# Optimization experiments

Measured on AMD Instinct MI355X. Metric: run time of the kernel, lower is better.

The kernel has to match this reference:

```python
import jax, jax.numpy as jnp
import numpy as np

N_NODES = 50000
N_EDGES = 800000
DIM_IN = 64
DIM_H = 32
HEADS = 4
NUM_CLASSES = 10
NEG_SLOPE = 0.2  # DGL GATv2Conv default negative_slope


def _gatv2_layer(x, W_src, b_src, W_dst, b_dst, attn, src, dst):
    """DGL GATv2Conv (share_weights=False, eval mode so feat_drop is identity).
    x: [N, F_in]; attn: [H, D]; returns [N, H, D]."""
    N = x.shape[0]
    H, D = attn.shape
    fs = (x @ W_src + b_src).reshape(N, H, D)  # source projection
    fd = (x @ W_dst + b_dst).reshape(N, H, D)  # destination projection
    # per-edge additive attention: leaky_relu(fs[u] + fd[v]) . attn  -> [E, H]
    e = jax.nn.leaky_relu(fs[src] + fd[dst], NEG_SLOPE)  # [E, H, D]
    s = jnp.einsum('ehd,hd->eh', e, attn)  # [E, H]
    # edge softmax over incoming edges of each destination node
    smax = jax.lax.stop_gradient(
        jax.ops.segment_max(s, dst, num_segments=N))  # [N, H]
    es = jnp.exp(s - smax[dst])
    denom = jax.ops.segment_sum(es, dst, num_segments=N)  # [N, H]
    alpha = es / denom[dst]
    # weighted scatter-aggregate of source features
    out = jax.ops.segment_sum(alpha[:, :, None] * fs[src], dst, num_segments=N)
    return out  # [N, H, D]


def setup_inputs() -> dict:
    key = jax.random.key(0)
    ks = jax.random.split(key, 16)
    sc = 0.05
    inp = {
        'g_feats': jax.random.normal(ks[0], (N_NODES, DIM_IN), jnp.float32),
        'edge_src': jax.random.randint(ks[1], (N_EDGES,), 0, N_NODES, jnp.int32),
        'edge_dst': jax.random.randint(ks[2], (N_EDGES,), 0, N_NODES, jnp.int32),
        # input embedding Linear(dim_in, dim_h)
        'W_in': jax.random.normal(ks[3], (DIM_IN, DIM_H), jnp.float32) * sc,
        'b_in': jnp.zeros((DIM_H,), jnp.float32),
        # GATv2 layer 1: Linear(dim_h, heads*dim_h) for src/dst + attn [H, D]
        'W1_src': jax.random.normal(ks[4], (DIM_H, HEADS * DIM_H), jnp.float32) * sc,
        'b1_src': jnp.zeros((HEADS * DIM_H,), jnp.float32),
        'W1_dst': jax.random.normal(ks[5], (DIM_H, HEADS * DIM_H), jnp.float32) * sc,
        'b1_dst': jnp.zeros((HEADS * DIM_H,), jnp.float32),
        'attn1': jax.random.normal(ks[6], (HEADS, DIM_H), jnp.float32) * sc,
        # GATv2 layer 2
        'W2_src': jax.random.normal(ks[7], (DIM_H, HEADS * DIM_H), jnp.float32) * sc,
        'b2_src': jnp.zeros((HEADS * DIM_H,), jnp.float32),
        'W2_dst': jax.random.normal(ks[8], (DIM_H, HEADS * DIM_H), jnp.float32) * sc,
        'b2_dst': jnp.zeros((HEADS * DIM_H,), jnp.float32),
        'attn2': jax.random.normal(ks[9], (HEADS, DIM_H), jnp.float32) * sc,
        # MLP head: Linear(dim_h, dim_h) -> relu -> (dropout: eval) -> Linear(dim_h, num_classes)
        'Wh1': jax.random.normal(ks[10], (DIM_H, DIM_H), jnp.float32) * sc,
        'bh1': jnp.zeros((DIM_H,), jnp.float32),
        'Wh2': jax.random.normal(ks[11], (DIM_H, NUM_CLASSES), jnp.float32) * sc,
        'bh2': jnp.zeros((NUM_CLASSES,), jnp.float32),
    }
    return inp


def reference(g_feats, W_in, b_in,
              W1_src, b1_src, W1_dst, b1_dst, attn1,
              W2_src, b2_src, W2_dst, b2_dst, attn2,
              Wh1, bh1, Wh2, bh2,
              edge_src, edge_dst):
    x = g_feats @ W_in + b_in  # input embedding, [N, dim_h]
    h = _gatv2_layer(x, W1_src, b1_src, W1_dst, b1_dst, attn1, edge_src, edge_dst)
    h = jax.nn.relu(h.mean(axis=1))  # mean over heads -> [N, dim_h]
    h = _gatv2_layer(h, W2_src, b2_src, W2_dst, b2_dst, attn2, edge_src, edge_dst)
    h = h.mean(axis=1)  # [N, dim_h]
    # dgl.readout_nodes(op='mean') over the single graph -> [1, dim_h]
    g = h.mean(axis=0, keepdims=True)
    g = jax.nn.relu(g @ Wh1 + bh1)  # head (dropout inactive in eval)
    logits = g @ Wh2 + bh2
    return jax.nn.softmax(logits, axis=-1)  # [1, num_classes]
```

## Files before the change

kernel.cpp:

```cpp
#include <hip/hip_runtime.h>
#include <hip/hip_bf16.h>

#define N_NODES 50000
#define N_EDGES 800000
#define DIM_IN 64
#define DIM_H 32
#define HEADS 4
#define NCLS 10
#define NEG 0.2f
#define NBUCK 196


__global__ void k_bhist(const int* __restrict__ dst, int* __restrict__ bh) {
    __shared__ int lh[NBUCK];
    for (int i = threadIdx.x; i < NBUCK; i += 256) lh[i] = 0;
    __syncthreads();
    int base = blockIdx.x * 1024 + threadIdx.x;
#pragma unroll
    for (int r = 0; r < 4; r++) {
        int e = base + r * 256;
        if (e < N_EDGES) atomicAdd(&lh[dst[e] >> 8], 1);
    }
    __syncthreads();
    for (int i = threadIdx.x; i < NBUCK; i += 256) {
        int c = lh[i];
        if (c) atomicAdd(&bh[i], c);
    }
}

__global__ void k_bscan(const int* __restrict__ bh, int* __restrict__ bbase,
                        int* __restrict__ gcur) {
    __shared__ int s[256];
    int t = threadIdx.x;
    int v = (t < NBUCK) ? bh[t] : 0;
    s[t] = v;
    __syncthreads();
    for (int off = 1; off < 256; off <<= 1) {
        int u = (t >= off) ? s[t - off] : 0;
        __syncthreads();
        s[t] += u;
        __syncthreads();
    }
    int excl = s[t] - v;
    if (t < NBUCK) {
        bbase[t] = excl;
        gcur[t] = excl;
    }
    if (t == 0) bbase[NBUCK] = N_EDGES;
}

__global__ void k_bin(const int* __restrict__ src, const int* __restrict__ dst,
                      int* __restrict__ gcur, unsigned* __restrict__ stage) {
    __shared__ int lh[NBUCK], chunk[NBUCK];
    int t = threadIdx.x;
    for (int i = t; i < NBUCK; i += 256) lh[i] = 0;
    __syncthreads();
    int e0 = blockIdx.x * 4096;
    unsigned pk[16];
    int bk[16];
#pragma unroll
    for (int r = 0; r < 16; r++) {
        int e = e0 + r * 256 + t;
        bool ok = e < N_EDGES;
        int s = ok ? src[e] : 0;
        int d = ok ? dst[e] : 0;
        bk[r] = ok ? (d >> 8) : -1;
        pk[r] = (unsigned)s | ((unsigned)(d & 255) << 16);
        if (ok) atomicAdd(&lh[bk[r]], 1);
    }
    __syncthreads();
    for (int i = t; i < NBUCK; i += 256) {
        int c = lh[i];
        chunk[i] = c ? atomicAdd(&gcur[i], c) : 0;
        lh[i] = 0;
    }
    __syncthreads();
#pragma unroll
    for (int r = 0; r < 16; r++) {
        if (bk[r] >= 0) {
            int lp = atomicAdd(&lh[bk[r]], 1);
            stage[chunk[bk[r]] + lp] = pk[r];
        }
    }
}

__global__ void k_csr(const unsigned* __restrict__ stage, const int* __restrict__ bbase,
                      int* __restrict__ row, int* __restrict__ adj) {
    __shared__ int lcnt[256], lcur[256], sc[256];
    int b = blockIdx.x, t = threadIdx.x;
    int s0 = bbase[b], s1 = bbase[b + 1];
    lcnt[t] = 0;
    __syncthreads();
    for (int i = s0 + t; i < s1; i += 256) atomicAdd(&lcnt[stage[i] >> 16], 1);
    __syncthreads();
    int v = lcnt[t];
    sc[t] = v;
    __syncthreads();
    for (int off = 1; off < 256; off <<= 1) {
        int u = (t >= off) ? sc[t - off] : 0;
        __syncthreads();
        sc[t] += u;
        __syncthreads();
    }
    int excl = sc[t] - v;
    int n = b * 256 + t;
    if (n < N_NODES) row[n] = s0 + excl;
    if (b == NBUCK - 1 && t == 0) row[N_NODES] = N_EDGES;
    lcur[t] = s0 + excl;
    __syncthreads();
    for (int i = s0 + t; i < s1; i += 256) {
        unsigned p = stage[i];
        int pos = atomicAdd(&lcur[p >> 16], 1);
        adj[pos] = (int)(p & 0xFFFFu);
    }
}


__device__ __forceinline__ unsigned short f2bf(float v) {
    unsigned u = __builtin_bit_cast(unsigned, v);
    u += 0x7FFFu + ((u >> 16) & 1u);
    return (unsigned short)(u >> 16);
}
__device__ __forceinline__ float bf2f(unsigned short h) {
    return __builtin_bit_cast(float, (unsigned)h << 16);
}

__global__ __launch_bounds__(256, 1) void k_fused1(
    const float* __restrict__ gf, const float* __restrict__ W_in,
    const float* __restrict__ b_in, const float* __restrict__ W1s,
    const float* __restrict__ b1s, const float* __restrict__ W1d,
    const float* __restrict__ b1d, unsigned short* __restrict__ fsh,
    float* __restrict__ fd) {
    __shared__ float4 xb[4][2][8];
    int lane = threadIdx.x & 63;
    int wvl = threadIdx.x >> 6;
    int wave = (blockIdx.x * 256 + threadIdx.x) >> 6;
    int c = lane & 31, h = lane >> 5;
    int n0 = wave * 16;
    if (n0 >= N_NODES) return;
    float wi[32];
#pragma unroll
    for (int k = 0; k < 32; k++) wi[k] = W_in[(h * 32 + k) * DIM_H + c];
    float bc = b_in[c];
    const float4* Wb = (lane < 32) ? (const float4*)W1s : (const float4*)W1d;
    const float4* bb = (lane < 32) ? (const float4*)b1s : (const float4*)b1d;
    float4 w[32];
#pragma unroll
    for (int k = 0; k < 32; k++) w[k] = Wb[k * 32 + c];
    float4 bias = bb[c];
#pragma unroll 2
    for (int i = 0; i < 16; i++) {
        int nu = __builtin_amdgcn_readfirstlane(n0 + i);
        const float4* gr = (const float4*)(gf + (size_t)nu * DIM_IN + h * 32);
        float a1 = 0.f;
#pragma unroll
        for (int k4 = 0; k4 < 8; k4++) {
            float4 xv = gr[k4];
            a1 += xv.x * wi[k4 * 4 + 0];
            a1 += xv.y * wi[k4 * 4 + 1];
            a1 += xv.z * wi[k4 * 4 + 2];
            a1 += xv.w * wi[k4 * 4 + 3];
        }
        a1 += __shfl_xor(a1, 32, 64);
        if (lane < 32) ((float*)&xb[wvl][i & 1][0])[c] = a1 + bc;
        float4 acc = bias;
#pragma unroll
        for (int k4 = 0; k4 < 8; k4++) {
            float4 xv = xb[wvl][i & 1][k4];
#pragma unroll
            for (int j = 0; j < 4; j++) {
                float xk = (j == 0) ? xv.x : (j == 1) ? xv.y : (j == 2) ? xv.z : xv.w;
                float4 wk = w[k4 * 4 + j];
                acc.x += xk * wk.x;
                acc.y += xk * wk.y;
                acc.z += xk * wk.z;
                acc.w += xk * wk.w;
            }
        }
        if (lane < 32) {
            ushort4 o;
            o.x = f2bf(acc.x);
            o.y = f2bf(acc.y);
            o.z = f2bf(acc.z);
            o.w = f2bf(acc.w);
            *(ushort4*)&fsh[(size_t)nu * 128 + c * 4] = o;
        } else {
            *(float4*)&fd[(size_t)nu * 128 + c * 4] = acc;
        }
    }
}

__global__ __launch_bounds__(256, 1) void k_proj(
    const float* __restrict__ x, const float* __restrict__ Wsrc,
    const float* __restrict__ bsrc, const float* __restrict__ Wdst,
    const float* __restrict__ bdst, unsigned short* __restrict__ fsh,
    float* __restrict__ fd) {
    int lane = threadIdx.x & 63;
    int wave = (blockIdx.x * 256 + threadIdx.x) >> 6;
    int cl = lane & 31;
    int n0 = wave * 16;
    if (n0 >= N_NODES) return;
    const float4* Wb = (lane < 32) ? (const float4*)Wsrc : (const float4*)Wdst;
    const float4* bb = (lane < 32) ? (const float4*)bsrc : (const float4*)bdst;
    float4 w[32];
#pragma unroll
    for (int k = 0; k < 32; k++) w[k] = Wb[k * 32 + cl];
    float4 bias = bb[cl];
#pragma unroll 2
    for (int i = 0; i < 16; i++) {
        int nu = __builtin_amdgcn_readfirstlane(n0 + i);
        const float4* xr = (const float4*)(x + (size_t)nu * DIM_H);
        float4 acc = bias;
#pragma unroll
        for (int k4 = 0; k4 < 8; k4++) {
            float4 xv = xr[k4];
#pragma unroll
            for (int j = 0; j < 4; j++) {
                float xk = (j == 0) ? xv.x : (j == 1) ? xv.y : (j == 2) ? xv.z : xv.w;
                float4 wk = w[k4 * 4 + j];
                acc.x += xk * wk.x;
                acc.y += xk * wk.y;
                acc.z += xk * wk.z;
                acc.w += xk * wk.w;
            }
        }
        if (lane < 32) {
            ushort4 o;
            o.x = f2bf(acc.x);
            o.y = f2bf(acc.y);
            o.z = f2bf(acc.z);
            o.w = f2bf(acc.w);
            *(ushort4*)&fsh[(size_t)nu * 128 + cl * 4] = o;
        } else {
            *(float4*)&fd[(size_t)nu * 128 + cl * 4] = acc;
        }
    }
}

__device__ __forceinline__ void pair_acc(const unsigned short* fsh, unsigned byteoff,
                                         float4 fdv, float4 a4, float4& acc,
                                         float& den, bool valid) {
    ushort4 u = *(const ushort4*)((const char*)fsh + byteoff);
    float f0 = bf2f(u.x), f1 = bf2f(u.y), f2 = bf2f(u.z), f3 = bf2f(u.w);
    float t0 = f0 + fdv.x; t0 = fmaxf(t0, NEG * t0);
    float t1 = f1 + fdv.y; t1 = fmaxf(t1, NEG * t1);
    float t2 = f2 + fdv.z; t2 = fmaxf(t2, NEG * t2);
    float t3 = f3 + fdv.w; t3 = fmaxf(t3, NEG * t3);
    float p = t0 * a4.x + t1 * a4.y + t2 * a4.z + t3 * a4.w;
    p += __shfl_xor(p, 1, 64);
    p += __shfl_xor(p, 2, 64);
    p += __shfl_xor(p, 4, 64);
    float w = __expf(p);
    if (!valid) w = 0.f;
    den += w;
    acc.x += w * f0;
    acc.y += w * f1;
    acc.z += w * f2;
    acc.w += w * f3;
}

__global__ void k_gather(const unsigned short* __restrict__ fsh,
                         const float* __restrict__ fd, const float* __restrict__ attn,
                         const int* __restrict__ row, const int* __restrict__ adj,
                         float* __restrict__ xout, int do_relu) {
    int wave = threadIdx.x >> 6;
    int lane = threadIdx.x & 63;
    int n = blockIdx.x * 4 + wave;
    if (n >= N_NODES) return;
    int sub = lane & 31, e2 = lane >> 5;
    unsigned suboff = (unsigned)sub << 3;
    float4 a4 = ((const float4*)attn)[sub];
    float4 fdv = ((const float4*)(fd + (size_t)n * 128))[sub];
    float4 acc = {0.f, 0.f, 0.f, 0.f};
    float den = 0.f;
    int beg = row[n], end = row[n + 1];
    for (int base = beg; base < end; base += 64) {
        int m = end - base;
        if (m > 64) m = 64;
        int myadj = (lane < m) ? adj[base + lane] : 0;
        int j = 0;
        for (; j + 8 <= m; j += 8) {
            unsigned o0 = ((unsigned)__shfl(myadj, j + 0 + e2, 64) << 8) + suboff;
            unsigned o1 = ((unsigned)__shfl(myadj, j + 2 + e2, 64) << 8) + suboff;
            unsigned o2 = ((unsigned)__shfl(myadj, j + 4 + e2, 64) << 8) + suboff;
            unsigned o3 = ((unsigned)__shfl(myadj, j + 6 + e2, 64) << 8) + suboff;
            pair_acc(fsh, o0, fdv, a4, acc, den, true);
            pair_acc(fsh, o1, fdv, a4, acc, den, true);
            pair_acc(fsh, o2, fdv, a4, acc, den, true);
            pair_acc(fsh, o3, fdv, a4, acc, den, true);
        }
        for (; j < m; j += 2) {
            int idx = j + e2;
            bool valid = idx < m;
            unsigned o = ((unsigned)__shfl(myadj, valid ? idx : j, 64) << 8) + suboff;
            pair_acc(fsh, o, fdv, a4, acc, den, valid);
        }
    }
    den += __shfl_xor(den, 32, 64);
    acc.x += __shfl_xor(acc.x, 32, 64);
    acc.y += __shfl_xor(acc.y, 32, 64);
    acc.z += __shfl_xor(acc.z, 32, 64);
    acc.w += __shfl_xor(acc.w, 32, 64);
    float inv = den > 0.f ? 0.25f / den : 0.f;
    float4 o;
    o.x = acc.x * inv;
    o.y = acc.y * inv;
    o.z = acc.z * inv;
    o.w = acc.w * inv;
    o.x += __shfl_xor(o.x, 8, 64);
    o.y += __shfl_xor(o.y, 8, 64);
    o.z += __shfl_xor(o.z, 8, 64);
    o.w += __shfl_xor(o.w, 8, 64);
    o.x += __shfl_xor(o.x, 16, 64);
    o.y += __shfl_xor(o.y, 16, 64);
    o.z += __shfl_xor(o.z, 16, 64);
    o.w += __shfl_xor(o.w, 16, 64);
    if (do_relu) {
        o.x = o.x > 0.f ? o.x : 0.f;
        o.y = o.y > 0.f ? o.y : 0.f;
        o.z = o.z > 0.f ? o.z : 0.f;
        o.w = o.w > 0.f ? o.w : 0.f;
    }
    if (lane < 8) ((float4*)(xout + (size_t)n * 32))[lane] = o;
}

__global__ void k_reduce(const float* __restrict__ x, float* __restrict__ partial) {
    int d = threadIdx.x & 31, g = threadIdx.x >> 5;
    float acc = 0.f;
    int stride = gridDim.x * 8;
    for (int n = blockIdx.x * 8 + g; n < N_NODES; n += stride) {
        acc += x[(size_t)n * 32 + d];
    }
    __shared__ float s[256];
    s[threadIdx.x] = acc;
    __syncthreads();
    for (int off = 128; off >= 32; off >>= 1) {
        if (threadIdx.x < off) s[threadIdx.x] += s[threadIdx.x + off];
        __syncthreads();
    }
    if (threadIdx.x < 32) partial[blockIdx.x * 32 + threadIdx.x] = s[threadIdx.x];
}

__global__ void k_final(const float* __restrict__ partial, const float* __restrict__ Wh1,
                        const float* __restrict__ bh1, const float* __restrict__ Wh2,
                        const float* __restrict__ bh2, float* __restrict__ out) {
    __shared__ float gv[32], gh[32], lg[16];
    int t = threadIdx.x;
    if (t < 32) {
        float s = 0.f;
        for (int b = 0; b < 256; b++) s += partial[b * 32 + t];
        gv[t] = s * (1.f / (float)N_NODES);
    }
    __syncthreads();
    if (t < 32) {
        float s = bh1[t];
        for (int d = 0; d < 32; d++) s += gv[d] * Wh1[d * 32 + t];
        gh[t] = s > 0.f ? s : 0.f;
    }
    __syncthreads();
    if (t < NCLS) {
        float s = bh2[t];
        for (int j = 0; j < 32; j++) s += gh[j] * Wh2[j * NCLS + t];
        lg[t] = s;
    }
    __syncthreads();
    if (t == 0) {
        float m = lg[0];
        for (int c = 1; c < NCLS; c++) m = fmaxf(m, lg[c]);
        float ex[NCLS], sum = 0.f;
        for (int c = 0; c < NCLS; c++) {
            ex[c] = __expf(lg[c] - m);
            sum += ex[c];
        }
        float inv = 1.f / sum;
        for (int c = 0; c < NCLS; c++) out[c] = ex[c] * inv;
    }
}

extern "C" void kernel_launch(void* const* d_in, const int* in_sizes, int n_in,
                              void* d_out, int out_size, void* d_ws, size_t ws_size,
                              hipStream_t stream) {
    const float* g_feats = (const float*)d_in[0];
    const int* edge_src = (const int*)d_in[1];
    const int* edge_dst = (const int*)d_in[2];
    const float* W_in = (const float*)d_in[3];
    const float* b_in = (const float*)d_in[4];
    const float* W1_src = (const float*)d_in[5];
    const float* b1_src = (const float*)d_in[6];
    const float* W1_dst = (const float*)d_in[7];
    const float* b1_dst = (const float*)d_in[8];
    const float* attn1 = (const float*)d_in[9];
    const float* W2_src = (const float*)d_in[10];
    const float* b2_src = (const float*)d_in[11];
    const float* W2_dst = (const float*)d_in[12];
    const float* b2_dst = (const float*)d_in[13];
    const float* attn2 = (const float*)d_in[14];
    const float* Wh1 = (const float*)d_in[15];
    const float* bh1 = (const float*)d_in[16];
    const float* Wh2 = (const float*)d_in[17];
    const float* bh2 = (const float*)d_in[18];

    float* x = (float*)d_ws;
    unsigned short* fsh = (unsigned short*)(x + (size_t)N_NODES * 32);
    float* fd = (float*)(fsh + (size_t)N_NODES * 128);
    float* partial = fd + (size_t)N_NODES * 128;
    int* row = (int*)(partial + 256 * 32);
    int* bh = row + N_NODES + 1;
    int* bbase = bh + NBUCK;
    int* gcur = bbase + NBUCK + 1;
    unsigned* stage = (unsigned*)(gcur + NBUCK);
    int* adj = (int*)(stage + N_EDGES);

    const int WB = (N_NODES + 63) / 64;

    hipMemsetAsync(bh, 0, NBUCK * sizeof(int), stream);
    k_bhist<<<(N_EDGES + 1023) / 1024, 256, 0, stream>>>(edge_dst, bh);
    k_bscan<<<1, 256, 0, stream>>>(bh, bbase, gcur);
    k_bin<<<(N_EDGES + 4095) / 4096, 256, 0, stream>>>(edge_src, edge_dst, gcur, stage);
    k_csr<<<NBUCK, 256, 0, stream>>>(stage, bbase, row, adj);

    k_fused1<<<WB, 256, 0, stream>>>(g_feats, W_in, b_in, W1_src, b1_src, W1_dst,
                                     b1_dst, fsh, fd);
    k_gather<<<(N_NODES + 3) / 4, 256, 0, stream>>>(fsh, fd, attn1, row, adj, x, 1);

    k_proj<<<WB, 256, 0, stream>>>(x, W2_src, b2_src, W2_dst, b2_dst, fsh, fd);
    k_gather<<<(N_NODES + 3) / 4, 256, 0, stream>>>(fsh, fd, attn2, row, adj, x, 0);

    k_reduce<<<256, 256, 0, stream>>>(x, partial);
    k_final<<<1, 256, 0, stream>>>(partial, Wh1, bh1, Wh2, bh2, (float*)d_out);
}
```

Measured before the change: 226.1 us.

## Widen gather loads to 16B, fuse graph readout into second gather, retune projection

The edge gather now has each lane load 8 bf16 values (uint4) instead of 4, so 4 edges are processed per wave step with one fewer shuffle level in the per-head dot product. The second-layer gather adds its per-node outputs into block shared memory and then into 64 global partial slots with atomics, which removes the separate reduce kernel and the write and reread of x. The projection kernels process 25 nodes per wave with launch bounds allowing 2 blocks per SM. The costs are float atomics, which make the summation order nondeterministic, and a larger per-lane register footprint in the gather.

After: 198.2 us. -12.4%, faster.

```diff
diff --git a/kernel.cpp b/kernel.cpp
--- a/kernel.cpp
+++ b/kernel.cpp
@@ -9,6 +9,7 @@
 #define NCLS 10
 #define NEG 0.2f
 #define NBUCK 196
+#define NPW 25
 
 
 __global__ void k_bhist(const int* __restrict__ dst, int* __restrict__ bh) {
@@ -121,11 +122,14 @@
     u += 0x7FFFu + ((u >> 16) & 1u);
     return (unsigned short)(u >> 16);
 }
-__device__ __forceinline__ float bf2f(unsigned short h) {
-    return __builtin_bit_cast(float, (unsigned)h << 16);
-}
-
-__global__ __launch_bounds__(256, 1) void k_fused1(
+__device__ __forceinline__ float bfLO(unsigned u) {
+    return __builtin_bit_cast(float, u << 16);
+}
+__device__ __forceinline__ float bfHI(unsigned u) {
+    return __builtin_bit_cast(float, u & 0xFFFF0000u);
+}
+
+__global__ __launch_bounds__(256, 2) void k_fused1(
     const float* __restrict__ gf, const float* __restrict__ W_in,
     const float* __restrict__ b_in, const float* __restrict__ W1s,
     const float* __restrict__ b1s, const float* __restrict__ W1d,
@@ -136,7 +140,7 @@
     int wvl = threadIdx.x >> 6;
     int wave = (blockIdx.x * 256 + threadIdx.x) >> 6;
     int c = lane & 31, h = lane >> 5;
-    int n0 = wave * 16;
+    int n0 = wave * NPW;
     if (n0 >= N_NODES) return;
     float wi[32];
 #pragma unroll
@@ -149,7 +153,7 @@
     for (int k = 0; k < 32; k++) w[k] = Wb[k * 32 + c];
     float4 bias = bb[c];
 #pragma unroll 2
-    for (int i = 0; i < 16; i++) {
+    for (int i = 0; i < NPW; i++) {
         int nu = __builtin_amdgcn_readfirstlane(n0 + i);
         const float4* gr = (const float4*)(gf + (size_t)nu * DIM_IN + h * 32);
         float a1 = 0.f;
@@ -190,7 +194,7 @@
     }
 }
 
-__global__ __launch_bounds__(256, 1) void k_proj(
+__global__ __launch_bounds__(256, 2) void k_proj(
     const float* __restrict__ x, const float* __restrict__ Wsrc,
     const float* __restrict__ bsrc, const float* __restrict__ Wdst,
     const float* __restrict__ bdst, unsigned short* __restrict__ fsh,
@@ -198,7 +202,7 @@
     int lane = threadIdx.x & 63;
     int wave = (blockIdx.x * 256 + threadIdx.x) >> 6;
     int cl = lane & 31;
-    int n0 = wave * 16;
+    int n0 = wave * NPW;
     if (n0 >= N_NODES) return;
     const float4* Wb = (lane < 32) ? (const float4*)Wsrc : (const float4*)Wdst;
     const float4* bb = (lane < 32) ? (const float4*)bsrc : (const float4*)bdst;
@@ -207,7 +211,7 @@
     for (int k = 0; k < 32; k++) w[k] = Wb[k * 32 + cl];
     float4 bias = bb[cl];
 #pragma unroll 2
-    for (int i = 0; i < 16; i++) {
+    for (int i = 0; i < NPW; i++) {
         int nu = __builtin_amdgcn_readfirstlane(n0 + i);
         const float4* xr = (const float4*)(x + (size_t)nu * DIM_H);
         float4 acc = bias;
@@ -237,41 +241,57 @@
     }
 }
 
-__device__ __forceinline__ void pair_acc(const unsigned short* fsh, unsigned byteoff,
-                                         float4 fdv, float4 a4, float4& acc,
-                                         float& den, bool valid) {
-    ushort4 u = *(const ushort4*)((const char*)fsh + byteoff);
-    float f0 = bf2f(u.x), f1 = bf2f(u.y), f2 = bf2f(u.z), f3 = bf2f(u.w);
-    float t0 = f0 + fdv.x; t0 = fmaxf(t0, NEG * t0);
-    float t1 = f1 + fdv.y; t1 = fmaxf(t1, NEG * t1);
-    float t2 = f2 + fdv.z; t2 = fmaxf(t2, NEG * t2);
-    float t3 = f3 + fdv.w; t3 = fmaxf(t3, NEG * t3);
-    float p = t0 * a4.x + t1 * a4.y + t2 * a4.z + t3 * a4.w;
+__device__ __forceinline__ void edge4(uint4 u, const float* a8, const float* f8d,
+                                      float* acc, float& den, bool valid) {
+    float f[8];
+    f[0] = bfLO(u.x); f[1] = bfHI(u.x);
+    f[2] = bfLO(u.y); f[3] = bfHI(u.y);
+    f[4] = bfLO(u.z); f[5] = bfHI(u.z);
+    f[6] = bfLO(u.w); f[7] = bfHI(u.w);
+    float p = 0.f;
+#pragma unroll
+    for (int j = 0; j < 8; j++) {
+        float t = f[j] + f8d[j];
+        t = fmaxf(t, NEG * t);
+        p += t * a8[j];
+    }
     p += __shfl_xor(p, 1, 64);
     p += __shfl_xor(p, 2, 64);
-    p += __shfl_xor(p, 4, 64);
     float w = __expf(p);
     if (!valid) w = 0.f;
     den += w;
-    acc.x += w * f0;
-    acc.y += w * f1;
-    acc.z += w * f2;
-    acc.w += w * f3;
+#pragma unroll
+    for (int j = 0; j < 8; j++) acc[j] += w * f[j];
 }
 
 __global__ void k_gather(const unsigned short* __restrict__ fsh,
                          const float* __restrict__ fd, const float* __restrict__ attn,
                          const int* __restrict__ row, const int* __restrict__ adj,
-                         float* __restrict__ xout, int do_relu) {
-    int wave = threadIdx.x >> 6;
-    int lane = threadIdx.x & 63;
+                         float* __restrict__ xout, float* __restrict__ gpart,
+                         int mode) {
+    __shared__ float bsum[32];
+    int tid = threadIdx.x;
+    if (mode) {
+        if (tid < 32) bsum[tid] = 0.f;
+        __syncthreads();
+    }
+    int wave = tid >> 6;
+    int lane = tid & 63;
     int n = blockIdx.x * 4 + wave;
-    if (n >= N_NODES) return;
-    int sub = lane & 31, e2 = lane >> 5;
-    unsigned suboff = (unsigned)sub << 3;
-    float4 a4 = ((const float4*)attn)[sub];
-    float4 fdv = ((const float4*)(fd + (size_t)n * 128))[sub];
-    float4 acc = {0.f, 0.f, 0.f, 0.f};
+    int sub = lane & 15, eps = lane >> 4;
+    unsigned suboff = (unsigned)sub << 4;
+    float a8[8], f8d[8];
+    {
+        const float4* ap = (const float4*)attn + sub * 2;
+        float4 t0 = ap[0], t1 = ap[1];
+        a8[0] = t0.x; a8[1] = t0.y; a8[2] = t0.z; a8[3] = t0.w;
+        a8[4] = t1.x; a8[5] = t1.y; a8[6] = t1.z; a8[7] = t1.w;
+        const float4* fp = (const float4*)(fd + (size_t)n * 128) + sub * 2;
+        float4 d0 = fp[0], d1 = fp[1];
+        f8d[0] = d0.x; f8d[1] = d0.y; f8d[2] = d0.z; f8d[3] = d0.w;
+        f8d[4] = d1.x; f8d[5] = d1.y; f8d[6] = d1.z; f8d[7] = d1.w;
+    }
+    float acc[8] = {0.f, 0.f, 0.f, 0.f, 0.f, 0.f, 0.f, 0.f};
     float den = 0.f;
     int beg = row[n], end = row[n + 1];
     for (int base = beg; base < end; base += 64) {
@@ -280,75 +300,66 @@
         int myadj = (lane < m) ? adj[base + lane] : 0;
         int j = 0;
         for (; j + 8 <= m; j += 8) {
-            unsigned o0 = ((unsigned)__shfl(myadj, j + 0 + e2, 64) << 8) + suboff;
-            unsigned o1 = ((unsigned)__shfl(myadj, j + 2 + e2, 64) << 8) + suboff;
-            unsigned o2 = ((unsigned)__shfl(myadj, j + 4 + e2, 64) << 8) + suboff;
-            unsigned o3 = ((unsigned)__shfl(myadj, j + 6 + e2, 64) << 8) + suboff;
-            pair_acc(fsh, o0, fdv, a4, acc, den, true);
-            pair_acc(fsh, o1, fdv, a4, acc, den, true);
-            pair_acc(fsh, o2, fdv, a4, acc, den, true);
-            pair_acc(fsh, o3, fdv, a4, acc, den, true);
-        }
-        for (; j < m; j += 2) {
-            int idx = j + e2;
+            unsigned oa = ((unsigned)__shfl(myadj, j + eps, 64) << 8) + suboff;
+            unsigned ob = ((unsigned)__shfl(myadj, j + 4 + eps, 64) << 8) + suboff;
+            uint4 ua = *(const uint4*)((const char*)fsh + oa);
+            uint4 ub = *(const uint4*)((const char*)fsh + ob);
+            edge4(ua, a8, f8d, acc, den, true);
+            edge4(ub, a8, f8d, acc, den, true);
+        }
+        for (; j < m; j += 4) {
+            int idx = j + eps;
             bool valid = idx < m;
             unsigned o = ((unsigned)__shfl(myadj, valid ? idx : j, 64) << 8) + suboff;
-            pair_acc(fsh, o, fdv, a4, acc, den, valid);
-        }
-    }
+            uint4 u = *(const uint4*)((const char*)fsh + o);
+            edge4(u, a8, f8d, acc, den, valid);
+        }
+    }
+    den += __shfl_xor(den, 16, 64);
     den += __shfl_xor(den, 32, 64);
-    acc.x += __shfl_xor(acc.x, 32, 64);
-    acc.y += __shfl_xor(acc.y, 32, 64);
-    acc.z += __shfl_xor(acc.z, 32, 64);
-    acc.w += __shfl_xor(acc.w, 32, 64);
-    float inv = den > 0.f ? 0.25f / den : 0.f;
-    float4 o;
-    o.x = acc.x * inv;
-    o.y = acc.y * inv;
-    o.z = acc.z * inv;
-    o.w = acc.w * inv;
-    o.x += __shfl_xor(o.x, 8, 64);
-    o.y += __shfl_xor(o.y, 8, 64);
-    o.z += __shfl_xor(o.z, 8, 64);
-    o.w += __shfl_xor(o.w, 8, 64);
-    o.x += __shfl_xor(o.x, 16, 64);
-    o.y += __shfl_xor(o.y, 16, 64);
-    o.z += __shfl_xor(o.z, 16, 64);
-    o.w += __shfl_xor(o.w, 16, 64);
-    if (do_relu) {
-        o.x = o.x > 0.f ? o.x : 0.f;
-        o.y = o.y > 0.f ? o.y : 0.f;
-        o.z = o.z > 0.f ? o.z : 0.f;
-        o.w = o.w > 0.f ? o.w : 0.f;
-    }
-    if (lane < 8) ((float4*)(xout + (size_t)n * 32))[lane] = o;
-}
-
-__global__ void k_reduce(const float* __restrict__ x, float* __restrict__ partial) {
-    int d = threadIdx.x & 31, g = threadIdx.x >> 5;
-    float acc = 0.f;
-    int stride = gridDim.x * 8;
-    for (int n = blockIdx.x * 8 + g; n < N_NODES; n += stride) {
-        acc += x[(size_t)n * 32 + d];
-    }
-    __shared__ float s[256];
-    s[threadIdx.x] = acc;
-    __syncthreads();
-    for (int off = 128; off >= 32; off >>= 1) {
-        if (threadIdx.x < off) s[threadIdx.x] += s[threadIdx.x + off];
-        __syncthreads();
-    }
-    if (threadIdx.x < 32) partial[blockIdx.x * 32 + threadIdx.x] = s[threadIdx.x];
-}
-
-__global__ void k_final(const float* __restrict__ partial, const float* __restrict__ Wh1,
+#pragma unroll
+    for (int j = 0; j < 8; j++) {
+        acc[j] += __shfl_xor(acc[j], 16, 64);
+        acc[j] += __shfl_xor(acc[j], 32, 64);
+    }
+    float inv = den > 0.f ? 1.f / den : 0.f;
+    float o[8];
+#pragma unroll
+    for (int j = 0; j < 8; j++) {
+        float v = acc[j] * inv;
+        v += __shfl_xor(v, 4, 64);
+        v += __shfl_xor(v, 8, 64);
+        o[j] = v * 0.25f;
+    }
+    if (mode == 0) {
+        if (lane < 4) {
+            float4 lo, hi;
+            lo.x = fmaxf(o[0], 0.f); lo.y = fmaxf(o[1], 0.f);
+            lo.z = fmaxf(o[2], 0.f); lo.w = fmaxf(o[3], 0.f);
+            hi.x = fmaxf(o[4], 0.f); hi.y = fmaxf(o[5], 0.f);
+            hi.z = fmaxf(o[6], 0.f); hi.w = fmaxf(o[7], 0.f);
+            float4* xp = (float4*)(xout + (size_t)n * 32 + lane * 8);
+            xp[0] = lo;
+            xp[1] = hi;
+        }
+    } else {
+        if (lane < 4) {
+#pragma unroll
+            for (int j = 0; j < 8; j++) atomicAdd(&bsum[lane * 8 + j], o[j]);
+        }
+        __syncthreads();
+        if (tid < 32) atomicAdd(&gpart[(blockIdx.x & 63) * 32 + tid], bsum[tid]);
+    }
+}
+
+__global__ void k_final(const float* __restrict__ gpart, const float* __restrict__ Wh1,
                         const float* __restrict__ bh1, const float* __restrict__ Wh2,
                         const float* __restrict__ bh2, float* __restrict__ out) {
     __shared__ float gv[32], gh[32], lg[16];
     int t = threadIdx.x;
     if (t < 32) {
         float s = 0.f;
-        for (int b = 0; b < 256; b++) s += partial[b * 32 + t];
+        for (int b = 0; b < 64; b++) s += gpart[b * 32 + t];
         gv[t] = s * (1.f / (float)N_NODES);
     }
     __syncthreads();
@@ -403,17 +414,18 @@
     float* x = (float*)d_ws;
     unsigned short* fsh = (unsigned short*)(x + (size_t)N_NODES * 32);
     float* fd = (float*)(fsh + (size_t)N_NODES * 128);
-    float* partial = fd + (size_t)N_NODES * 128;
-    int* row = (int*)(partial + 256 * 32);
-    int* bh = row + N_NODES + 1;
+    float* gpart = fd + (size_t)N_NODES * 128;
+    int* bh = (int*)(gpart + 64 * 32);
     int* bbase = bh + NBUCK;
     int* gcur = bbase + NBUCK + 1;
-    unsigned* stage = (unsigned*)(gcur + NBUCK);
+    int* row = gcur + NBUCK;
+    unsigned* stage = (unsigned*)(row + N_NODES + 1);
     int* adj = (int*)(stage + N_EDGES);
 
-    const int WB = (N_NODES + 63) / 64;
-
-    hipMemsetAsync(bh, 0, NBUCK * sizeof(int), stream);
+    const int WB = (N_NODES / NPW + 3) / 4;
+
+    hipMemsetAsync(gpart, 0, (64 * 32 + NBUCK) * sizeof(int), stream);
+
     k_bhist<<<(N_EDGES + 1023) / 1024, 256, 0, stream>>>(edge_dst, bh);
     k_bscan<<<1, 256, 0, stream>>>(bh, bbase, gcur);
     k_bin<<<(N_EDGES + 4095) / 4096, 256, 0, stream>>>(edge_src, edge_dst, gcur, stage);
@@ -421,11 +433,10 @@
 
     k_fused1<<<WB, 256, 0, stream>>>(g_feats, W_in, b_in, W1_src, b1_src, W1_dst,
                                      b1_dst, fsh, fd);
-    k_gather<<<(N_NODES + 3) / 4, 256, 0, stream>>>(fsh, fd, attn1, row, adj, x, 1);
+    k_gather<<<N_NODES / 4, 256, 0, stream>>>(fsh, fd, attn1, row, adj, x, gpart, 0);
 
     k_proj<<<WB, 256, 0, stream>>>(x, W2_src, b2_src, W2_dst, b2_dst, fsh, fd);
-    k_gather<<<(N_NODES + 3) / 4, 256, 0, stream>>>(fsh, fd, attn2, row, adj, x, 0);
-
-    k_reduce<<<256, 256, 0, stream>>>(x, partial);
-    k_final<<<1, 256, 0, stream>>>(partial, Wh1, bh1, Wh2, bh2, (float*)d_out);
-}
+    k_gather<<<N_NODES / 4, 256, 0, stream>>>(fsh, fd, attn2, row, adj, x, gpart, 1);
+
+    k_final<<<1, 256, 0, stream>>>(gpart, Wh1, bh1, Wh2, bh2, (float*)d_out);
+}
```
